# Kernel optimization log

Hardware: AMD Instinct MI355X
Metric: run time of the kernel (lower is better)

## Reference

```python
import jax, jax.numpy as jnp
import numpy as np

B, NV, HID, TDIM = 1024, 256, 256, 128
NODE_IN = 2 + 4 + TDIM  # coords + pos_enc(4) + time_emb


def _sinusoidal_pos_emb(t, dim):
    # standard SinusoidalPosEmb: cat(sin, cos) of t * exp(-i*log(1e4)/(half-1))
    half = dim // 2
    freqs = jnp.exp(-np.log(10000.0) * jnp.arange(half, dtype=t.dtype) / (half - 1))
    ang = t[:, None] * freqs[None, :]
    return jnp.concatenate([jnp.sin(ang), jnp.cos(ang)], axis=-1)  # [B, dim]


def setup_inputs() -> dict:
    key = jax.random.key(0)
    ks = jax.random.split(key, 10)
    s = lambda fan_in: 1.0 / np.sqrt(fan_in)
    return {
        "x": jax.random.normal(ks[0], (B, NV * 2), dtype=jnp.float32),
        "t": jax.random.uniform(ks[1], (B,), dtype=jnp.float32) * 1000.0,
        "time_w": jax.random.normal(ks[2], (TDIM, TDIM), dtype=jnp.float32) * s(TDIM),
        "time_b": jnp.zeros((TDIM,), dtype=jnp.float32),
        "W0": jax.random.normal(ks[3], (NODE_IN, HID), dtype=jnp.float32) * s(NODE_IN),
        "b0": jnp.zeros((HID,), dtype=jnp.float32),
        "W1": jax.random.normal(ks[4], (HID, HID), dtype=jnp.float32) * s(HID),
        "b1": jnp.zeros((HID,), dtype=jnp.float32),
        "W2": jax.random.normal(ks[5], (HID, HID), dtype=jnp.float32) * s(HID),
        "b2": jnp.zeros((HID,), dtype=jnp.float32),
    }


def reference(x, t, time_w, time_b, W0, b0, W1, b1, W2, b2):
    Bsz, D = x.shape
    n = D // 2
    coords = x.reshape(Bsz, n, 2)  # [B, n, 2]

    # cycle positional features (pos_enc_dim=4): sin/cos of vertex angle + 2nd harmonic
    pos = jnp.arange(n, dtype=x.dtype)
    theta = (2.0 * jnp.pi) * pos / n
    pe = jnp.stack([jnp.sin(theta), jnp.cos(theta), jnp.sin(2.0 * theta), jnp.cos(2.0 * theta)], axis=-1)
    pe = jnp.broadcast_to(pe[None], (Bsz, n, 4))

    # time MLP: SinusoidalPosEmb -> Linear -> SiLU, broadcast to every node of the graph
    temb = jax.nn.silu(_sinusoidal_pos_emb(t, time_w.shape[0]) @ time_w + time_b)  # [B, TDIM]
    temb = jnp.broadcast_to(temb[:, None, :], (Bsz, n, temb.shape[-1]))

    h = jnp.concatenate([coords, pe, temb], axis=-1)  # [B, n, NODE_IN]

    # GCN layers over cycle adjacency with self-loops, symmetric-normalized (deg=3 -> 1/3).
    # Cycle structure: neighbors are prev/next vertex within each polygon -> jnp.roll on axis 1.
    for W, b in ((W0, b0), (W1, b1), (W2, b2)):
        s = h @ W + b  # support = x W + b
        agg = (s + jnp.roll(s, 1, axis=1) + jnp.roll(s, -1, axis=1)) / 3.0
        h = jax.nn.silu(agg)

    # mean pooling per graph (scatter_mean over graph_index == mean over vertex axis here)
    return h.mean(axis=1)  # [B, HID]
```

## Files before the change

kernel.cpp:

```cpp
#include <hip/hip_runtime.h>
#include <cstdint>

typedef __attribute__((ext_vector_type(8)))  short bf16x8;
typedef __attribute__((ext_vector_type(16))) float f32x16;
typedef __attribute__((ext_vector_type(2)))  float f32x2;
typedef __attribute__((ext_vector_type(4)))  int   i32x4;

__device__ __forceinline__ unsigned short f2bf(float x) {
  unsigned u = __float_as_uint(x);
  u += 0x7fffu + ((u >> 16) & 1u);
  return (unsigned short)(u >> 16);
}
__device__ __forceinline__ float bf2f(unsigned short h) {
  return __uint_as_float(((unsigned)h) << 16);
}
__device__ __forceinline__ float silu_f(float v) {
  return v * __builtin_amdgcn_rcpf(1.0f + __expf(-v));
}
__device__ __forceinline__ unsigned pk2bf(float lo, float hi) {
#if defined(__has_builtin)
#if __has_builtin(__builtin_amdgcn_cvt_pk_bf16_f32)
  auto v = __builtin_amdgcn_cvt_pk_bf16_f32(lo, hi);
  unsigned u; __builtin_memcpy(&u, &v, 4); return u;
#else
  return ((unsigned)f2bf(hi) << 16) | (unsigned)f2bf(lo);
#endif
#else
  return ((unsigned)f2bf(hi) << 16) | (unsigned)f2bf(lo);
#endif
}
__device__ __forceinline__ unsigned lo_pack(unsigned x, unsigned y) {
  return __builtin_amdgcn_perm(y, x, 0x05040100u);
}
__device__ __forceinline__ unsigned hi_pack(unsigned x, unsigned y) {
  return __builtin_amdgcn_perm(y, x, 0x07060302u);
}

__global__ void pack_kernel(const float* __restrict__ W0, const float* __restrict__ W1,
                            const float* __restrict__ W2,
                            unsigned short* __restrict__ packW) {
  __shared__ float ldsF[16][257];
  const int s = blockIdx.x, tid = threadIdx.x;
  const float* W; int KT, kmax, base, kt;
  if (s < 9)       { W = W0; KT = 9;  kmax = 134; base = 0;      kt = s; }
  else if (s < 25) { W = W1; KT = 16; kmax = 256; base = 36864;  kt = s - 9; }
  else             { W = W2; KT = 16; kmax = 256; base = 102400; kt = s - 25; }
  const int k0 = kt * 16;
#pragma unroll
  for (int i = 0; i < 8; ++i) {
    const int idx = i * 512 + tid;
    const int kl = idx >> 8, col = idx & 255;
    const int kg = k0 + kl;
    ldsF[kl][col] = (kg < kmax) ? W[kg * 256 + col] : 0.0f;
  }
  __syncthreads();
  const int g = tid >> 7, t = (tid >> 6) & 1, lane = tid & 63;
  const int col = g * 64 + t * 32 + (lane & 31);
  const int kb = 8 * (lane >> 5);
  unsigned u0 = pk2bf(ldsF[kb + 0][col], ldsF[kb + 1][col]);
  unsigned u1 = pk2bf(ldsF[kb + 2][col], ldsF[kb + 3][col]);
  unsigned u2 = pk2bf(ldsF[kb + 4][col], ldsF[kb + 5][col]);
  unsigned u3 = pk2bf(ldsF[kb + 6][col], ldsF[kb + 7][col]);
  unsigned short* dst = packW + base + g * (KT * 1024) + t * (KT * 512) + kt * 512 + lane * 8;
  i32x4 v = { (int)u0, (int)u1, (int)u2, (int)u3 };
  *(i32x4*)dst = v;
}

template <int KT, int LAYER>
__device__ __forceinline__ void gcn_layer(
    const int w, const int lane, const int q, const int c, const int sig,
    const int wp, const int wn, const int ebase,
    const unsigned short* __restrict__ packL,
    const float* __restrict__ BIAS,
    const bf16x8* Aold, bf16x8* Anew,
    unsigned short* bndE, unsigned int* flagsL,
    unsigned int* scr3_w, float* poolw) {
#pragma unroll
  for (int g = 0; g < 4; ++g) {
    const int e = ebase + g;
    const unsigned short* srcg = packL + g * (KT * 1024);

    f32x16 acc0, acc1;
#pragma unroll
    for (int i = 0; i < 16; ++i) { acc0[i] = 0.f; acc1[i] = 0.f; }
    {
      const bf16x8* wb0 = (const bf16x8*)srcg;
      const bf16x8* wb1 = (const bf16x8*)(srcg + KT * 512);
#pragma unroll
      for (int kt = 0; kt < KT; ++kt) {
        bf16x8 b0 = wb0[kt * 64 + lane];
        bf16x8 b1 = wb1[kt * 64 + lane];
        acc0 = __builtin_amdgcn_mfma_f32_32x32x16_bf16(Aold[kt], b0, acc0, 0, 0, 0);
        acc1 = __builtin_amdgcn_mfma_f32_32x32x16_bf16(Aold[kt], b1, acc1, 0, 0, 0);
      }
    }

    {
      unsigned short* myb = bndE + (e * 8 + w) * 128;
      if (q == 0) { myb[c]      = f2bf(acc0[0]);  myb[32 + c] = f2bf(acc1[0]);  }
      else        { myb[64 + c] = f2bf(acc0[15]); myb[96 + c] = f2bf(acc1[15]); }
      if (lane == 0)
        __hip_atomic_store(&flagsL[e * 8 + w], 1u, __ATOMIC_RELEASE,
                           __HIP_MEMORY_SCOPE_WORKGROUP);
    }

    const float e0t0  = __shfl_xor(acc0[0], 32);
    const float e0t1  = __shfl_xor(acc1[0], 32);
    const float e15t0 = __shfl_xor(acc0[15], 32);
    const float e15t1 = __shfl_xor(acc1[15], 32);

#pragma clang loop unroll(disable)
    while (__hip_atomic_load(&flagsL[e * 8 + wp], __ATOMIC_ACQUIRE,
                             __HIP_MEMORY_SCOPE_WORKGROUP) == 0u)
      __builtin_amdgcn_s_sleep(1);
#pragma clang loop unroll(disable)
    while (__hip_atomic_load(&flagsL[e * 8 + wn], __ATOMIC_ACQUIRE,
                             __HIP_MEMORY_SCOPE_WORKGROUP) == 0u)
      __builtin_amdgcn_s_sleep(1);

    const float bp0 = bf2f(bndE[(e * 8 + wp) * 128 + 64 + c]);
    const float bp1 = bf2f(bndE[(e * 8 + wp) * 128 + 96 + c]);
    const float bn0 = bf2f(bndE[(e * 8 + wn) * 128 + c]);
    const float bn1 = bf2f(bndE[(e * 8 + wn) * 128 + 32 + c]);
    const float bias0 = BIAS[g * 64 + c], bias1 = BIAS[g * 64 + 32 + c];
    const float T = 0.33333333333f;
    float ps0 = 0.f, ps1 = 0.f;
#pragma unroll
    for (int r = 0; r < 16; ++r) {
      float pr0, pr1, nx0, nx1;
      if (r > 0)       { pr0 = acc0[r - 1]; pr1 = acc1[r - 1]; }
      else             { pr0 = q ? e15t0 : bp0; pr1 = q ? e15t1 : bp1; }
      if (r < 15)      { nx0 = acc0[r + 1]; nx1 = acc1[r + 1]; }
      else             { nx0 = q ? bn0 : e0t0; nx1 = q ? bn1 : e0t1; }
      f32x2 v2;
      v2.x = (pr0 + acc0[r] + nx0) * T + bias0;
      v2.y = (pr1 + acc1[r] + nx1) * T + bias1;
      f32x2 ex; ex.x = __expf(-v2.x); ex.y = __expf(-v2.y);
      f32x2 den = ex + 1.0f;
      f32x2 y2;
      y2.x = v2.x * __builtin_amdgcn_rcpf(den.x);
      y2.y = v2.y * __builtin_amdgcn_rcpf(den.y);
      if constexpr (LAYER == 2) { ps0 += y2.x; ps1 += y2.y; }
      else {
        scr3_w[(16 * q + r) * 34 + c] = pk2bf(y2.x, y2.y);
      }
    }

    if constexpr (LAYER == 2) {
      ps0 += __shfl_xor(ps0, 32);
      ps1 += __shfl_xor(ps1, 32);
      if (q == 0) { poolw[w * 256 + g * 64 + c]      = ps0;
                    poolw[w * 256 + g * 64 + 32 + c] = ps1; }
    } else {
      const unsigned int* sb = scr3_w + sig * 34;
      uint2 d0 = *(const uint2*)(sb + 8 * q + 0);
      uint2 d1 = *(const uint2*)(sb + 8 * q + 2);
      uint2 d2 = *(const uint2*)(sb + 8 * q + 4);
      uint2 d3 = *(const uint2*)(sb + 8 * q + 6);
      uint2 e0 = *(const uint2*)(sb + 16 + 8 * q + 0);
      uint2 e1 = *(const uint2*)(sb + 16 + 8 * q + 2);
      uint2 e2 = *(const uint2*)(sb + 16 + 8 * q + 4);
      uint2 e3 = *(const uint2*)(sb + 16 + 8 * q + 6);
      i32x4 f0 = { (int)lo_pack(d0.x, d0.y), (int)lo_pack(d1.x, d1.y),
                   (int)lo_pack(d2.x, d2.y), (int)lo_pack(d3.x, d3.y) };
      i32x4 f1 = { (int)lo_pack(e0.x, e0.y), (int)lo_pack(e1.x, e1.y),
                   (int)lo_pack(e2.x, e2.y), (int)lo_pack(e3.x, e3.y) };
      i32x4 f2v = { (int)hi_pack(d0.x, d0.y), (int)hi_pack(d1.x, d1.y),
                    (int)hi_pack(d2.x, d2.y), (int)hi_pack(d3.x, d3.y) };
      i32x4 f3 = { (int)hi_pack(e0.x, e0.y), (int)hi_pack(e1.x, e1.y),
                   (int)hi_pack(e2.x, e2.y), (int)hi_pack(e3.x, e3.y) };
      Anew[g * 4 + 0] = __builtin_bit_cast(bf16x8, f0);
      Anew[g * 4 + 1] = __builtin_bit_cast(bf16x8, f1);
      Anew[g * 4 + 2] = __builtin_bit_cast(bf16x8, f2v);
      Anew[g * 4 + 3] = __builtin_bit_cast(bf16x8, f3);
    }
  }
}

__global__ __launch_bounds__(512, 2) void poly_kernel(
    const float* __restrict__ x, const float* __restrict__ t,
    const float* __restrict__ tw, const float* __restrict__ tb,
    const unsigned short* __restrict__ packW,
    const float* __restrict__ B0, const float* __restrict__ B1,
    const float* __restrict__ B2, float* __restrict__ out) {
  __shared__ __align__(16) unsigned short bndE[12288];
  __shared__ unsigned int flagsL[96];
  __shared__ __align__(16) unsigned int   scr3[8 * 1088];
  __shared__ float poolL[2048];
  __shared__ __align__(16) unsigned short temb_sh[160];

  const int tid = threadIdx.x;
  const int w = tid >> 6, lane = tid & 63;
  const int q = lane >> 5, c = lane & 31;
  const int wp = (w + 7) & 7, wn = (w + 1) & 7;
  const int b = blockIdx.x;
  const int sig = (c & 3) + 4 * ((c >> 3) & 3) + 16 * ((c >> 2) & 1);

  if (lane < 12) flagsL[lane * 8 + w] = 0;

  {
    float* e_sh = (float*)bndE;
    float* part = (float*)scr3;
    if (tid < 128) {
      const float tv = t[b];
      const int i = tid & 63;
      const float f = expf(-0.14619588396823767f * (float)i);
      const float ang = tv * f;
      e_sh[tid] = (tid < 64) ? sinf(ang) : cosf(ang);
    }
    __syncthreads();
    {
      const int j = tid & 127, p = tid >> 7;
      float a = 0.f;
#pragma unroll 8
      for (int kk = 0; kk < 32; ++kk) {
        const int k = p * 32 + kk;
        a += e_sh[k] * tw[k * 128 + j];
      }
      part[tid] = a;
    }
    __syncthreads();
    if (tid < 128) {
      const float a = tb[tid] + part[tid] + part[128 + tid] + part[256 + tid] + part[384 + tid];
      temb_sh[6 + tid] = f2bf(silu_f(a));
      if (tid < 6)  temb_sh[tid] = 0;
      if (tid < 10) temb_sh[134 + tid] = 0;
    }
    __syncthreads();
  }

  bf16x8 A0[9], A1[16], A2[16];
  {
#pragma unroll
    for (int kt = 0; kt < 9; ++kt)
      A0[kt] = *(const bf16x8*)(temb_sh + kt * 16 + q * 8);
    if (q == 0) {
      const int n = w * 32 + sig;
      const float2 xy = ((const float2*)x)[b * 256 + n];
      const float th = 0.024543692605870074f * (float)n;
      A0[0][0] = (short)f2bf(xy.x);
      A0[0][1] = (short)f2bf(xy.y);
      A0[0][2] = (short)f2bf(sinf(th));
      A0[0][3] = (short)f2bf(cosf(th));
      A0[0][4] = (short)f2bf(sinf(2.f * th));
      A0[0][5] = (short)f2bf(cosf(2.f * th));
    }
  }

  unsigned int* scr3_w = scr3 + w * 1088;
  gcn_layer< 9, 0>(w, lane, q, c, sig, wp, wn, 0, packW,          B0, A0, A1,
                   bndE, flagsL, scr3_w, poolL);
  gcn_layer<16, 1>(w, lane, q, c, sig, wp, wn, 4, packW + 36864,  B1, A1, A2,
                   bndE, flagsL, scr3_w, poolL);
  gcn_layer<16, 2>(w, lane, q, c, sig, wp, wn, 8, packW + 102400, B2, A2, A1,
                   bndE, flagsL, scr3_w, poolL);

  __syncthreads();
  if (tid < 256) {
    float s = 0.f;
#pragma unroll
    for (int ww = 0; ww < 8; ++ww) s += poolL[ww * 256 + tid];
    out[b * 256 + tid] = s * (1.f / 256.f);
  }
}

extern "C" void kernel_launch(void* const* d_in, const int* in_sizes, int n_in,
                              void* d_out, int out_size, void* d_ws, size_t ws_size,
                              hipStream_t stream) {
  const float* x  = (const float*)d_in[0];
  const float* t  = (const float*)d_in[1];
  const float* tw = (const float*)d_in[2];
  const float* tb = (const float*)d_in[3];
  const float* W0 = (const float*)d_in[4];
  const float* b0 = (const float*)d_in[5];
  const float* W1 = (const float*)d_in[6];
  const float* b1 = (const float*)d_in[7];
  const float* W2 = (const float*)d_in[8];
  const float* b2 = (const float*)d_in[9];

  unsigned short* packW = (unsigned short*)d_ws;
  float* out = (float*)d_out;

  pack_kernel<<<41, 512, 0, stream>>>(W0, W1, W2, packW);
  poly_kernel<<<1024, 512, 0, stream>>>(x, t, tw, tb, packW, b0, b1, b2, out);
}
```

Measured before the change: 211.1 us.

## Software-pipeline GCN epilogue of previous column group with next group's MFMAs

Restructures each GCN layer so the stencil/SiLU epilogue of column group g-1 is interleaved with the MFMA k-loop of group g, using double-buffered accumulators. Weight B-fragments are also prefetched two k-steps ahead. The aim is to hide epilogue ALU/transcendental work and LDS boundary exchange behind matrix-core latency. In exchange it holds two sets of accumulators live, which raises VGPR pressure under launch_bounds(512,2) and risks spills or lower occupancy.

```diff
diff --git a/kernel.cpp b/kernel.cpp
--- a/kernel.cpp
+++ b/kernel.cpp
@@ -3,7 +3,6 @@
 
 typedef __attribute__((ext_vector_type(8)))  short bf16x8;
 typedef __attribute__((ext_vector_type(16))) float f32x16;
-typedef __attribute__((ext_vector_type(2)))  float f32x2;
 typedef __attribute__((ext_vector_type(4)))  int   i32x4;
 
 __device__ __forceinline__ unsigned short f2bf(float x) {
@@ -13,9 +12,6 @@
 }
 __device__ __forceinline__ float bf2f(unsigned short h) {
   return __uint_as_float(((unsigned)h) << 16);
-}
-__device__ __forceinline__ float silu_f(float v) {
-  return v * __builtin_amdgcn_rcpf(1.0f + __expf(-v));
 }
 __device__ __forceinline__ unsigned pk2bf(float lo, float hi) {
 #if defined(__has_builtin)
@@ -29,6 +25,9 @@
   return ((unsigned)f2bf(hi) << 16) | (unsigned)f2bf(lo);
 #endif
 }
+__device__ __forceinline__ float silu_f(float v) {
+  return v * __builtin_amdgcn_rcpf(1.0f + __expf(-v));
+}
 __device__ __forceinline__ unsigned lo_pack(unsigned x, unsigned y) {
   return __builtin_amdgcn_perm(y, x, 0x05040100u);
 }
@@ -66,6 +65,10 @@
   *(i32x4*)dst = v;
 }
 
+struct EpiPre {
+  float e0t0, e0t1, e15t0, e15t1, bp0, bp1, bn0, bn1, bias0, bias1;
+};
+
 template <int KT, int LAYER>
 __device__ __forceinline__ void gcn_layer(
     const int w, const int lane, const int q, const int c, const int sig,
@@ -75,82 +78,54 @@
     const bf16x8* Aold, bf16x8* Anew,
     unsigned short* bndE, unsigned int* flagsL,
     unsigned int* scr3_w, float* poolw) {
-#pragma unroll
-  for (int g = 0; g < 4; ++g) {
-    const int e = ebase + g;
-    const unsigned short* srcg = packL + g * (KT * 1024);
-
-    f32x16 acc0, acc1;
-#pragma unroll
-    for (int i = 0; i < 16; ++i) { acc0[i] = 0.f; acc1[i] = 0.f; }
-    {
-      const bf16x8* wb0 = (const bf16x8*)srcg;
-      const bf16x8* wb1 = (const bf16x8*)(srcg + KT * 512);
-#pragma unroll
-      for (int kt = 0; kt < KT; ++kt) {
-        bf16x8 b0 = wb0[kt * 64 + lane];
-        bf16x8 b1 = wb1[kt * 64 + lane];
-        acc0 = __builtin_amdgcn_mfma_f32_32x32x16_bf16(Aold[kt], b0, acc0, 0, 0, 0);
-        acc1 = __builtin_amdgcn_mfma_f32_32x32x16_bf16(Aold[kt], b1, acc1, 0, 0, 0);
-      }
-    }
-
-    {
-      unsigned short* myb = bndE + (e * 8 + w) * 128;
-      if (q == 0) { myb[c]      = f2bf(acc0[0]);  myb[32 + c] = f2bf(acc1[0]);  }
-      else        { myb[64 + c] = f2bf(acc0[15]); myb[96 + c] = f2bf(acc1[15]); }
-      if (lane == 0)
-        __hip_atomic_store(&flagsL[e * 8 + w], 1u, __ATOMIC_RELEASE,
-                           __HIP_MEMORY_SCOPE_WORKGROUP);
-    }
-
-    const float e0t0  = __shfl_xor(acc0[0], 32);
-    const float e0t1  = __shfl_xor(acc1[0], 32);
-    const float e15t0 = __shfl_xor(acc0[15], 32);
-    const float e15t1 = __shfl_xor(acc1[15], 32);
-
-#pragma clang loop unroll(disable)
-    while (__hip_atomic_load(&flagsL[e * 8 + wp], __ATOMIC_ACQUIRE,
+  const float T = 0.33333333333f;
+  f32x16 a0[2], a1[2];
+  EpiPre ep;
+  float ps0 = 0.f, ps1 = 0.f;
+
+  auto spin = [&](int ww, int e) {
+    while (__hip_atomic_load(&flagsL[e * 8 + ww], __ATOMIC_ACQUIRE,
                              __HIP_MEMORY_SCOPE_WORKGROUP) == 0u)
       __builtin_amdgcn_s_sleep(1);
-#pragma clang loop unroll(disable)
-    while (__hip_atomic_load(&flagsL[e * 8 + wn], __ATOMIC_ACQUIRE,
-                             __HIP_MEMORY_SCOPE_WORKGROUP) == 0u)
-      __builtin_amdgcn_s_sleep(1);
-
-    const float bp0 = bf2f(bndE[(e * 8 + wp) * 128 + 64 + c]);
-    const float bp1 = bf2f(bndE[(e * 8 + wp) * 128 + 96 + c]);
-    const float bn0 = bf2f(bndE[(e * 8 + wn) * 128 + c]);
-    const float bn1 = bf2f(bndE[(e * 8 + wn) * 128 + 32 + c]);
-    const float bias0 = BIAS[g * 64 + c], bias1 = BIAS[g * 64 + 32 + c];
-    const float T = 0.33333333333f;
-    float ps0 = 0.f, ps1 = 0.f;
-#pragma unroll
-    for (int r = 0; r < 16; ++r) {
-      float pr0, pr1, nx0, nx1;
-      if (r > 0)       { pr0 = acc0[r - 1]; pr1 = acc1[r - 1]; }
-      else             { pr0 = q ? e15t0 : bp0; pr1 = q ? e15t1 : bp1; }
-      if (r < 15)      { nx0 = acc0[r + 1]; nx1 = acc1[r + 1]; }
-      else             { nx0 = q ? bn0 : e0t0; nx1 = q ? bn1 : e0t1; }
-      f32x2 v2;
-      v2.x = (pr0 + acc0[r] + nx0) * T + bias0;
-      v2.y = (pr1 + acc1[r] + nx1) * T + bias1;
-      f32x2 ex; ex.x = __expf(-v2.x); ex.y = __expf(-v2.y);
-      f32x2 den = ex + 1.0f;
-      f32x2 y2;
-      y2.x = v2.x * __builtin_amdgcn_rcpf(den.x);
-      y2.y = v2.y * __builtin_amdgcn_rcpf(den.y);
-      if constexpr (LAYER == 2) { ps0 += y2.x; ps1 += y2.y; }
-      else {
-        scr3_w[(16 * q + r) * 34 + c] = pk2bf(y2.x, y2.y);
-      }
-    }
-
+  };
+  auto publish = [&](int g, const f32x16& C0, const f32x16& C1) {
+    unsigned short* myb = bndE + ((ebase + g) * 8 + w) * 128;
+    if (q == 0) { myb[c]      = f2bf(C0[0]);  myb[32 + c] = f2bf(C1[0]);  }
+    else        { myb[64 + c] = f2bf(C0[15]); myb[96 + c] = f2bf(C1[15]); }
+    if (lane == 0)
+      __hip_atomic_store(&flagsL[(ebase + g) * 8 + w], 1u, __ATOMIC_RELEASE,
+                         __HIP_MEMORY_SCOPE_WORKGROUP);
+  };
+  auto epi_prep = [&](int pg, const f32x16& P0, const f32x16& P1) {
+    const int e = ebase + pg;
+    ep.e0t0  = __shfl_xor(P0[0], 32);  ep.e0t1  = __shfl_xor(P1[0], 32);
+    ep.e15t0 = __shfl_xor(P0[15], 32); ep.e15t1 = __shfl_xor(P1[15], 32);
+    ep.bp0 = bf2f(bndE[(e * 8 + wp) * 128 + 64 + c]);
+    ep.bp1 = bf2f(bndE[(e * 8 + wp) * 128 + 96 + c]);
+    ep.bn0 = bf2f(bndE[(e * 8 + wn) * 128 + c]);
+    ep.bn1 = bf2f(bndE[(e * 8 + wn) * 128 + 32 + c]);
+    ep.bias0 = BIAS[pg * 64 + c]; ep.bias1 = BIAS[pg * 64 + 32 + c];
+    ps0 = 0.f; ps1 = 0.f;
+  };
+  auto epi_iter = [&](int r, const f32x16& P0, const f32x16& P1) {
+    float pr0, pr1, nx0, nx1;
+    if (r > 0)  { pr0 = P0[r - 1]; pr1 = P1[r - 1]; }
+    else        { pr0 = q ? ep.e15t0 : ep.bp0; pr1 = q ? ep.e15t1 : ep.bp1; }
+    if (r < 15) { nx0 = P0[r + 1]; nx1 = P1[r + 1]; }
+    else        { nx0 = q ? ep.bn0 : ep.e0t0; nx1 = q ? ep.bn1 : ep.e0t1; }
+    const float v0 = (pr0 + P0[r] + nx0) * T + ep.bias0;
+    const float v1 = (pr1 + P1[r] + nx1) * T + ep.bias1;
+    const float y0 = silu_f(v0);
+    const float y1 = silu_f(v1);
+    if constexpr (LAYER == 2) { ps0 += y0; ps1 += y1; }
+    else scr3_w[(16 * q + r) * 34 + c] = pk2bf(y0, y1);
+  };
+  auto epi_fini = [&](int pg) {
     if constexpr (LAYER == 2) {
-      ps0 += __shfl_xor(ps0, 32);
-      ps1 += __shfl_xor(ps1, 32);
-      if (q == 0) { poolw[w * 256 + g * 64 + c]      = ps0;
-                    poolw[w * 256 + g * 64 + 32 + c] = ps1; }
+      float s0 = ps0 + __shfl_xor(ps0, 32);
+      float s1 = ps1 + __shfl_xor(ps1, 32);
+      if (q == 0) { poolw[w * 256 + pg * 64 + c]      = s0;
+                    poolw[w * 256 + pg * 64 + 32 + c] = s1; }
     } else {
       const unsigned int* sb = scr3_w + sig * 34;
       uint2 d0 = *(const uint2*)(sb + 8 * q + 0);
@@ -169,12 +144,52 @@
                     (int)hi_pack(d2.x, d2.y), (int)hi_pack(d3.x, d3.y) };
       i32x4 f3 = { (int)hi_pack(e0.x, e0.y), (int)hi_pack(e1.x, e1.y),
                    (int)hi_pack(e2.x, e2.y), (int)hi_pack(e3.x, e3.y) };
-      Anew[g * 4 + 0] = __builtin_bit_cast(bf16x8, f0);
-      Anew[g * 4 + 1] = __builtin_bit_cast(bf16x8, f1);
-      Anew[g * 4 + 2] = __builtin_bit_cast(bf16x8, f2v);
-      Anew[g * 4 + 3] = __builtin_bit_cast(bf16x8, f3);
-    }
-  }
+      Anew[pg * 4 + 0] = __builtin_bit_cast(bf16x8, f0);
+      Anew[pg * 4 + 1] = __builtin_bit_cast(bf16x8, f1);
+      Anew[pg * 4 + 2] = __builtin_bit_cast(bf16x8, f2v);
+      Anew[pg * 4 + 3] = __builtin_bit_cast(bf16x8, f3);
+    }
+  };
+  auto run_group = [&](int g, f32x16& C0, f32x16& C1,
+                       const f32x16& P0, const f32x16& P1, bool doEpi) {
+    const bf16x8* wb0 = (const bf16x8*)(packL + g * (KT * 1024));
+    const bf16x8* wb1 = (const bf16x8*)(packL + g * (KT * 1024) + KT * 512);
+#pragma unroll
+    for (int i = 0; i < 16; ++i) { C0[i] = 0.f; C1[i] = 0.f; }
+    bf16x8 pb0[2], pb1[2];
+    pb0[0] = wb0[lane]; pb1[0] = wb1[lane];
+    if (KT > 1) { pb0[1] = wb0[64 + lane]; pb1[1] = wb1[64 + lane]; }
+#pragma unroll
+    for (int kt = 0; kt < KT; ++kt) {
+      bf16x8 b0 = pb0[kt & 1], b1 = pb1[kt & 1];
+      if (kt + 2 < KT) { pb0[kt & 1] = wb0[(kt + 2) * 64 + lane];
+                         pb1[kt & 1] = wb1[(kt + 2) * 64 + lane]; }
+      C0 = __builtin_amdgcn_mfma_f32_32x32x16_bf16(Aold[kt], b0, C0, 0, 0, 0);
+      C1 = __builtin_amdgcn_mfma_f32_32x32x16_bf16(Aold[kt], b1, C1, 0, 0, 0);
+      if (doEpi) {
+#pragma unroll
+        for (int r = (kt * 16) / KT; r < ((kt + 1) * 16) / KT; ++r)
+          epi_iter(r, P0, P1);
+      }
+    }
+  };
+
+  run_group(0, a0[0], a1[0], a0[0], a1[0], false);
+  publish(0, a0[0], a1[0]);
+#pragma unroll
+  for (int g = 1; g <= 3; ++g) {
+    const int pg = g - 1, pp = pg & 1, cp = g & 1;
+    spin(wp, ebase + pg); spin(wn, ebase + pg);
+    epi_prep(pg, a0[pp], a1[pp]);
+    run_group(g, a0[cp], a1[cp], a0[pp], a1[pp], true);
+    epi_fini(pg);
+    publish(g, a0[cp], a1[cp]);
+  }
+  spin(wp, ebase + 3); spin(wn, ebase + 3);
+  epi_prep(3, a0[1], a1[1]);
+#pragma unroll
+  for (int r = 0; r < 16; ++r) epi_iter(r, a0[1], a1[1]);
+  epi_fini(3);
 }
 
 __global__ __launch_bounds__(512, 2) void poly_kernel(
```

New measurement: 201.9 us. -4.3%, faster.

## Compute all output column tiles per layer at once with one neighbor sync

Applied to the files above, without the earlier changes.

Each GCN layer now issues MFMAs for all eight 32-column tiles in a single k-loop, holding eight accumulators instead of two per column group. The prev/next boundary rows are then exchanged through LDS with one flag handshake per layer instead of four. The weight pack layout is reordered to match this k-major, tile-inner order. The layer-1 activations are rewritten in place, and the pooling buffer and time-embedding scratch now reuse the boundary LDS region, which cuts register arrays and LDS footprint. The cost is 128 accumulator floats live per lane, which may cause spills or lower occupancy under the 512x2 launch bounds.

```diff
diff --git a/kernel.cpp b/kernel.cpp
--- a/kernel.cpp
+++ b/kernel.cpp
@@ -3,7 +3,6 @@
 
 typedef __attribute__((ext_vector_type(8)))  short bf16x8;
 typedef __attribute__((ext_vector_type(16))) float f32x16;
-typedef __attribute__((ext_vector_type(2)))  float f32x2;
 typedef __attribute__((ext_vector_type(4)))  int   i32x4;
 
 __device__ __forceinline__ unsigned short f2bf(float x) {
@@ -13,9 +12,6 @@
 }
 __device__ __forceinline__ float bf2f(unsigned short h) {
   return __uint_as_float(((unsigned)h) << 16);
-}
-__device__ __forceinline__ float silu_f(float v) {
-  return v * __builtin_amdgcn_rcpf(1.0f + __expf(-v));
 }
 __device__ __forceinline__ unsigned pk2bf(float lo, float hi) {
 #if defined(__has_builtin)
@@ -29,6 +25,9 @@
   return ((unsigned)f2bf(hi) << 16) | (unsigned)f2bf(lo);
 #endif
 }
+__device__ __forceinline__ float silu_f(float v) {
+  return v * __builtin_amdgcn_rcpf(1.0f + __expf(-v));
+}
 __device__ __forceinline__ unsigned lo_pack(unsigned x, unsigned y) {
   return __builtin_amdgcn_perm(y, x, 0x05040100u);
 }
@@ -41,10 +40,10 @@
                             unsigned short* __restrict__ packW) {
   __shared__ float ldsF[16][257];
   const int s = blockIdx.x, tid = threadIdx.x;
-  const float* W; int KT, kmax, base, kt;
-  if (s < 9)       { W = W0; KT = 9;  kmax = 134; base = 0;      kt = s; }
-  else if (s < 25) { W = W1; KT = 16; kmax = 256; base = 36864;  kt = s - 9; }
-  else             { W = W2; KT = 16; kmax = 256; base = 102400; kt = s - 25; }
+  const float* W; int kmax, base, kt;
+  if (s < 9)       { W = W0; kmax = 134; base = 0;      kt = s; }
+  else if (s < 25) { W = W1; kmax = 256; base = 36864;  kt = s - 9; }
+  else             { W = W2; kmax = 256; base = 102400; kt = s - 25; }
   const int k0 = kt * 16;
 #pragma unroll
   for (int i = 0; i < 8; ++i) {
@@ -54,103 +53,101 @@
     ldsF[kl][col] = (kg < kmax) ? W[kg * 256 + col] : 0.0f;
   }
   __syncthreads();
-  const int g = tid >> 7, t = (tid >> 6) & 1, lane = tid & 63;
-  const int col = g * 64 + t * 32 + (lane & 31);
+  const int j = tid >> 6, lane = tid & 63;
+  const int col = j * 32 + (lane & 31);
   const int kb = 8 * (lane >> 5);
-  unsigned u0 = pk2bf(ldsF[kb + 0][col], ldsF[kb + 1][col]);
-  unsigned u1 = pk2bf(ldsF[kb + 2][col], ldsF[kb + 3][col]);
-  unsigned u2 = pk2bf(ldsF[kb + 4][col], ldsF[kb + 5][col]);
-  unsigned u3 = pk2bf(ldsF[kb + 6][col], ldsF[kb + 7][col]);
-  unsigned short* dst = packW + base + g * (KT * 1024) + t * (KT * 512) + kt * 512 + lane * 8;
-  i32x4 v = { (int)u0, (int)u1, (int)u2, (int)u3 };
-  *(i32x4*)dst = v;
+  i32x4 v = { (int)pk2bf(ldsF[kb + 0][col], ldsF[kb + 1][col]),
+              (int)pk2bf(ldsF[kb + 2][col], ldsF[kb + 3][col]),
+              (int)pk2bf(ldsF[kb + 4][col], ldsF[kb + 5][col]),
+              (int)pk2bf(ldsF[kb + 6][col], ldsF[kb + 7][col]) };
+  *(i32x4*)(packW + base + (kt * 8 + j) * 512 + lane * 8) = v;
 }
 
 template <int KT, int LAYER>
 __device__ __forceinline__ void gcn_layer(
     const int w, const int lane, const int q, const int c, const int sig,
-    const int wp, const int wn, const int ebase,
+    const int wp, const int wn, const int e,
     const unsigned short* __restrict__ packL,
     const float* __restrict__ BIAS,
     const bf16x8* Aold, bf16x8* Anew,
     unsigned short* bndE, unsigned int* flagsL,
     unsigned int* scr3_w, float* poolw) {
-#pragma unroll
-  for (int g = 0; g < 4; ++g) {
-    const int e = ebase + g;
-    const unsigned short* srcg = packL + g * (KT * 1024);
-
-    f32x16 acc0, acc1;
-#pragma unroll
-    for (int i = 0; i < 16; ++i) { acc0[i] = 0.f; acc1[i] = 0.f; }
-    {
-      const bf16x8* wb0 = (const bf16x8*)srcg;
-      const bf16x8* wb1 = (const bf16x8*)(srcg + KT * 512);
-#pragma unroll
-      for (int kt = 0; kt < KT; ++kt) {
-        bf16x8 b0 = wb0[kt * 64 + lane];
-        bf16x8 b1 = wb1[kt * 64 + lane];
-        acc0 = __builtin_amdgcn_mfma_f32_32x32x16_bf16(Aold[kt], b0, acc0, 0, 0, 0);
-        acc1 = __builtin_amdgcn_mfma_f32_32x32x16_bf16(Aold[kt], b1, acc1, 0, 0, 0);
+  const float T = 0.33333333333f;
+  f32x16 acc[8];
+#pragma unroll
+  for (int j = 0; j < 8; ++j)
+#pragma unroll
+    for (int i = 0; i < 16; ++i) acc[j][i] = 0.f;
+
+  {
+    const bf16x8* wb = (const bf16x8*)packL;
+#pragma unroll
+    for (int kt = 0; kt < KT; ++kt) {
+#pragma unroll
+      for (int j = 0; j < 8; ++j) {
+        bf16x8 bf = wb[(kt * 8 + j) * 64 + lane];
+        acc[j] = __builtin_amdgcn_mfma_f32_32x32x16_bf16(Aold[kt], bf, acc[j], 0, 0, 0);
       }
     }
-
-    {
-      unsigned short* myb = bndE + (e * 8 + w) * 128;
-      if (q == 0) { myb[c]      = f2bf(acc0[0]);  myb[32 + c] = f2bf(acc1[0]);  }
-      else        { myb[64 + c] = f2bf(acc0[15]); myb[96 + c] = f2bf(acc1[15]); }
-      if (lane == 0)
-        __hip_atomic_store(&flagsL[e * 8 + w], 1u, __ATOMIC_RELEASE,
-                           __HIP_MEMORY_SCOPE_WORKGROUP);
-    }
-
-    const float e0t0  = __shfl_xor(acc0[0], 32);
-    const float e0t1  = __shfl_xor(acc1[0], 32);
-    const float e15t0 = __shfl_xor(acc0[15], 32);
-    const float e15t1 = __shfl_xor(acc1[15], 32);
-
+  }
+
+  {
+    unsigned short* myb = bndE + (e * 8 + w) * 512;
+    if (q == 0) {
+#pragma unroll
+      for (int j = 0; j < 8; ++j) myb[j * 32 + c] = f2bf(acc[j][0]);
+    } else {
+#pragma unroll
+      for (int j = 0; j < 8; ++j) myb[256 + j * 32 + c] = f2bf(acc[j][15]);
+    }
+    if (lane == 0)
+      __hip_atomic_store(&flagsL[e * 8 + w], 1u, __ATOMIC_RELEASE,
+                         __HIP_MEMORY_SCOPE_WORKGROUP);
+  }
 #pragma clang loop unroll(disable)
-    while (__hip_atomic_load(&flagsL[e * 8 + wp], __ATOMIC_ACQUIRE,
-                             __HIP_MEMORY_SCOPE_WORKGROUP) == 0u)
-      __builtin_amdgcn_s_sleep(1);
+  while (__hip_atomic_load(&flagsL[e * 8 + wp], __ATOMIC_ACQUIRE,
+                           __HIP_MEMORY_SCOPE_WORKGROUP) == 0u)
+    __builtin_amdgcn_s_sleep(1);
 #pragma clang loop unroll(disable)
-    while (__hip_atomic_load(&flagsL[e * 8 + wn], __ATOMIC_ACQUIRE,
-                             __HIP_MEMORY_SCOPE_WORKGROUP) == 0u)
-      __builtin_amdgcn_s_sleep(1);
-
-    const float bp0 = bf2f(bndE[(e * 8 + wp) * 128 + 64 + c]);
-    const float bp1 = bf2f(bndE[(e * 8 + wp) * 128 + 96 + c]);
-    const float bn0 = bf2f(bndE[(e * 8 + wn) * 128 + c]);
-    const float bn1 = bf2f(bndE[(e * 8 + wn) * 128 + 32 + c]);
-    const float bias0 = BIAS[g * 64 + c], bias1 = BIAS[g * 64 + 32 + c];
-    const float T = 0.33333333333f;
+  while (__hip_atomic_load(&flagsL[e * 8 + wn], __ATOMIC_ACQUIRE,
+                           __HIP_MEMORY_SCOPE_WORKGROUP) == 0u)
+    __builtin_amdgcn_s_sleep(1);
+
+  const unsigned short* pb = bndE + (e * 8 + wp) * 512 + 256;
+  const unsigned short* nb = bndE + (e * 8 + wn) * 512;
+
+#pragma unroll
+  for (int cg = 0; cg < 4; ++cg) {
+    const int j0 = 2 * cg, j1 = 2 * cg + 1;
+    const float e0t0  = __shfl_xor(acc[j0][0], 32);
+    const float e0t1  = __shfl_xor(acc[j1][0], 32);
+    const float e15t0 = __shfl_xor(acc[j0][15], 32);
+    const float e15t1 = __shfl_xor(acc[j1][15], 32);
+    const float bp0 = bf2f(pb[j0 * 32 + c]);
+    const float bp1 = bf2f(pb[j1 * 32 + c]);
+    const float bn0 = bf2f(nb[j0 * 32 + c]);
+    const float bn1 = bf2f(nb[j1 * 32 + c]);
+    const float bias0 = BIAS[j0 * 32 + c], bias1 = BIAS[j1 * 32 + c];
     float ps0 = 0.f, ps1 = 0.f;
 #pragma unroll
     for (int r = 0; r < 16; ++r) {
       float pr0, pr1, nx0, nx1;
-      if (r > 0)       { pr0 = acc0[r - 1]; pr1 = acc1[r - 1]; }
-      else             { pr0 = q ? e15t0 : bp0; pr1 = q ? e15t1 : bp1; }
-      if (r < 15)      { nx0 = acc0[r + 1]; nx1 = acc1[r + 1]; }
-      else             { nx0 = q ? bn0 : e0t0; nx1 = q ? bn1 : e0t1; }
-      f32x2 v2;
-      v2.x = (pr0 + acc0[r] + nx0) * T + bias0;
-      v2.y = (pr1 + acc1[r] + nx1) * T + bias1;
-      f32x2 ex; ex.x = __expf(-v2.x); ex.y = __expf(-v2.y);
-      f32x2 den = ex + 1.0f;
-      f32x2 y2;
-      y2.x = v2.x * __builtin_amdgcn_rcpf(den.x);
-      y2.y = v2.y * __builtin_amdgcn_rcpf(den.y);
-      if constexpr (LAYER == 2) { ps0 += y2.x; ps1 += y2.y; }
-      else {
-        scr3_w[(16 * q + r) * 34 + c] = pk2bf(y2.x, y2.y);
-      }
-    }
-
+      if (r > 0)  { pr0 = acc[j0][r - 1]; pr1 = acc[j1][r - 1]; }
+      else        { pr0 = q ? e15t0 : bp0; pr1 = q ? e15t1 : bp1; }
+      if (r < 15) { nx0 = acc[j0][r + 1]; nx1 = acc[j1][r + 1]; }
+      else        { nx0 = q ? bn0 : e0t0; nx1 = q ? bn1 : e0t1; }
+      const float v0 = (pr0 + acc[j0][r] + nx0) * T + bias0;
+      const float v1 = (pr1 + acc[j1][r] + nx1) * T + bias1;
+      const float y0 = silu_f(v0);
+      const float y1 = silu_f(v1);
+      if constexpr (LAYER == 2) { ps0 += y0; ps1 += y1; }
+      else scr3_w[(16 * q + r) * 34 + c] = pk2bf(y0, y1);
+    }
     if constexpr (LAYER == 2) {
-      ps0 += __shfl_xor(ps0, 32);
-      ps1 += __shfl_xor(ps1, 32);
-      if (q == 0) { poolw[w * 256 + g * 64 + c]      = ps0;
-                    poolw[w * 256 + g * 64 + 32 + c] = ps1; }
+      float s0 = ps0 + __shfl_xor(ps0, 32);
+      float s1 = ps1 + __shfl_xor(ps1, 32);
+      if (q == 0) { poolw[w * 256 + cg * 64 + c]      = s0;
+                    poolw[w * 256 + cg * 64 + 32 + c] = s1; }
     } else {
       const unsigned int* sb = scr3_w + sig * 34;
       uint2 d0 = *(const uint2*)(sb + 8 * q + 0);
@@ -169,10 +166,10 @@
                     (int)hi_pack(d2.x, d2.y), (int)hi_pack(d3.x, d3.y) };
       i32x4 f3 = { (int)hi_pack(e0.x, e0.y), (int)hi_pack(e1.x, e1.y),
                    (int)hi_pack(e2.x, e2.y), (int)hi_pack(e3.x, e3.y) };
-      Anew[g * 4 + 0] = __builtin_bit_cast(bf16x8, f0);
-      Anew[g * 4 + 1] = __builtin_bit_cast(bf16x8, f1);
-      Anew[g * 4 + 2] = __builtin_bit_cast(bf16x8, f2v);
-      Anew[g * 4 + 3] = __builtin_bit_cast(bf16x8, f3);
+      Anew[cg * 4 + 0] = __builtin_bit_cast(bf16x8, f0);
+      Anew[cg * 4 + 1] = __builtin_bit_cast(bf16x8, f1);
+      Anew[cg * 4 + 2] = __builtin_bit_cast(bf16x8, f2v);
+      Anew[cg * 4 + 3] = __builtin_bit_cast(bf16x8, f3);
     }
   }
 }
@@ -184,10 +181,10 @@
     const float* __restrict__ B0, const float* __restrict__ B1,
     const float* __restrict__ B2, float* __restrict__ out) {
   __shared__ __align__(16) unsigned short bndE[12288];
-  __shared__ unsigned int flagsL[96];
+  __shared__ unsigned int flagsL[24];
   __shared__ __align__(16) unsigned int   scr3[8 * 1088];
-  __shared__ float poolL[2048];
   __shared__ __align__(16) unsigned short temb_sh[160];
+  float* poolL = (float*)bndE;
 
   const int tid = threadIdx.x;
   const int w = tid >> 6, lane = tid & 63;
@@ -196,10 +193,10 @@
   const int b = blockIdx.x;
   const int sig = (c & 3) + 4 * ((c >> 3) & 3) + 16 * ((c >> 2) & 1);
 
-  if (lane < 12) flagsL[lane * 8 + w] = 0;
-
-  {
-    float* e_sh = (float*)bndE;
+  if (lane < 3) flagsL[lane * 8 + w] = 0;
+
+  {
+    float* e_sh = (float*)(bndE + 4096);
     float* part = (float*)scr3;
     if (tid < 128) {
       const float tv = t[b];
@@ -229,7 +226,7 @@
     __syncthreads();
   }
 
-  bf16x8 A0[9], A1[16], A2[16];
+  bf16x8 A0[9], A1[16];
   {
 #pragma unroll
     for (int kt = 0; kt < 9; ++kt)
@@ -250,9 +247,9 @@
   unsigned int* scr3_w = scr3 + w * 1088;
   gcn_layer< 9, 0>(w, lane, q, c, sig, wp, wn, 0, packW,          B0, A0, A1,
                    bndE, flagsL, scr3_w, poolL);
-  gcn_layer<16, 1>(w, lane, q, c, sig, wp, wn, 4, packW + 36864,  B1, A1, A2,
+  gcn_layer<16, 1>(w, lane, q, c, sig, wp, wn, 1, packW + 36864,  B1, A1, A1,
                    bndE, flagsL, scr3_w, poolL);
-  gcn_layer<16, 2>(w, lane, q, c, sig, wp, wn, 8, packW + 102400, B2, A2, A1,
+  gcn_layer<16, 2>(w, lane, q, c, sig, wp, wn, 2, packW + 102400, B2, A1, A1,
                    bndE, flagsL, scr3_w, poolL);
 
   __syncthreads();
```

After: 319.8 us. +51.5%, slower.

## Replace flag spin-waits with double-buffered barrier exchange, prefetch weights, fold SiLU constants

Applied to the files above, without the earlier changes.

Each GCN group's neighbour-boundary exchange now uses a double-buffered LDS array of packed bf16 pairs and a single __syncthreads, replacing per-wave release/acquire flags and sleep-polling. This removes the flag and bndE LDS arrays and lets the pooling buffer alias the scratch array. The first weight fragment of the next group is prefetched into registers while the current group's epilogue runs. SiLU is rewritten with exp2 and pre-folded log2e, 1/3 and bias constants using paired float ops. The workgroup-wide barrier makes every wave wait for the slowest one in each group, where the old scheme only waited on the two neighbours.

```diff
diff --git a/kernel.cpp b/kernel.cpp
--- a/kernel.cpp
+++ b/kernel.cpp
@@ -13,9 +13,6 @@
 }
 __device__ __forceinline__ float bf2f(unsigned short h) {
   return __uint_as_float(((unsigned)h) << 16);
-}
-__device__ __forceinline__ float silu_f(float v) {
-  return v * __builtin_amdgcn_rcpf(1.0f + __expf(-v));
 }
 __device__ __forceinline__ unsigned pk2bf(float lo, float hi) {
 #if defined(__has_builtin)
@@ -28,6 +25,20 @@
 #else
   return ((unsigned)f2bf(hi) << 16) | (unsigned)f2bf(lo);
 #endif
+}
+__device__ __forceinline__ float exp2_f(float x) {
+#if defined(__has_builtin)
+#if __has_builtin(__builtin_amdgcn_exp2f)
+  return __builtin_amdgcn_exp2f(x);
+#else
+  return __builtin_exp2f(x);
+#endif
+#else
+  return __builtin_exp2f(x);
+#endif
+}
+__device__ __forceinline__ float silu_f(float v) {
+  return v * __builtin_amdgcn_rcpf(1.0f + __expf(-v));
 }
 __device__ __forceinline__ unsigned lo_pack(unsigned x, unsigned y) {
   return __builtin_amdgcn_perm(y, x, 0x05040100u);
@@ -69,25 +80,30 @@
 template <int KT, int LAYER>
 __device__ __forceinline__ void gcn_layer(
     const int w, const int lane, const int q, const int c, const int sig,
-    const int wp, const int wn, const int ebase,
     const unsigned short* __restrict__ packL,
     const float* __restrict__ BIAS,
     const bf16x8* Aold, bf16x8* Anew,
-    unsigned short* bndE, unsigned int* flagsL,
-    unsigned int* scr3_w, float* poolw) {
+    unsigned int* bndu, unsigned int* scr3_w, float* poolw) {
+  const float T  = 0.33333333333f;
+  const float L2E = 1.44269504f;
+  const float NL2 = -0.69314718f;
+
+  bf16x8 pf0 = ((const bf16x8*)packL)[lane];
+  bf16x8 pf1 = ((const bf16x8*)(packL + KT * 512))[lane];
+
 #pragma unroll
   for (int g = 0; g < 4; ++g) {
-    const int e = ebase + g;
     const unsigned short* srcg = packL + g * (KT * 1024);
-
     f32x16 acc0, acc1;
 #pragma unroll
     for (int i = 0; i < 16; ++i) { acc0[i] = 0.f; acc1[i] = 0.f; }
     {
       const bf16x8* wb0 = (const bf16x8*)srcg;
       const bf16x8* wb1 = (const bf16x8*)(srcg + KT * 512);
-#pragma unroll
-      for (int kt = 0; kt < KT; ++kt) {
+      acc0 = __builtin_amdgcn_mfma_f32_32x32x16_bf16(Aold[0], pf0, acc0, 0, 0, 0);
+      acc1 = __builtin_amdgcn_mfma_f32_32x32x16_bf16(Aold[0], pf1, acc1, 0, 0, 0);
+#pragma unroll
+      for (int kt = 1; kt < KT; ++kt) {
         bf16x8 b0 = wb0[kt * 64 + lane];
         bf16x8 b1 = wb1[kt * 64 + lane];
         acc0 = __builtin_amdgcn_mfma_f32_32x32x16_bf16(Aold[kt], b0, acc0, 0, 0, 0);
@@ -95,62 +111,55 @@
       }
     }
 
-    {
-      unsigned short* myb = bndE + (e * 8 + w) * 128;
-      if (q == 0) { myb[c]      = f2bf(acc0[0]);  myb[32 + c] = f2bf(acc1[0]);  }
-      else        { myb[64 + c] = f2bf(acc0[15]); myb[96 + c] = f2bf(acc1[15]); }
-      if (lane == 0)
-        __hip_atomic_store(&flagsL[e * 8 + w], 1u, __ATOMIC_RELEASE,
-                           __HIP_MEMORY_SCOPE_WORKGROUP);
-    }
+    if (g < 3) {
+      const unsigned short* nxt = packL + (g + 1) * (KT * 1024);
+      pf0 = ((const bf16x8*)nxt)[lane];
+      pf1 = ((const bf16x8*)(nxt + KT * 512))[lane];
+    }
+
+    unsigned int* bndp = bndu + (g & 1) * 1024;
+    if (q == 0) bndp[(w * 2 + 0) * 32 + c] = pk2bf(acc0[0],  acc1[0]);
+    else        bndp[(w * 2 + 1) * 32 + c] = pk2bf(acc0[15], acc1[15]);
+    __syncthreads();
 
     const float e0t0  = __shfl_xor(acc0[0], 32);
     const float e0t1  = __shfl_xor(acc1[0], 32);
     const float e15t0 = __shfl_xor(acc0[15], 32);
     const float e15t1 = __shfl_xor(acc1[15], 32);
-
-#pragma clang loop unroll(disable)
-    while (__hip_atomic_load(&flagsL[e * 8 + wp], __ATOMIC_ACQUIRE,
-                             __HIP_MEMORY_SCOPE_WORKGROUP) == 0u)
-      __builtin_amdgcn_s_sleep(1);
-#pragma clang loop unroll(disable)
-    while (__hip_atomic_load(&flagsL[e * 8 + wn], __ATOMIC_ACQUIRE,
-                             __HIP_MEMORY_SCOPE_WORKGROUP) == 0u)
-      __builtin_amdgcn_s_sleep(1);
-
-    const float bp0 = bf2f(bndE[(e * 8 + wp) * 128 + 64 + c]);
-    const float bp1 = bf2f(bndE[(e * 8 + wp) * 128 + 96 + c]);
-    const float bn0 = bf2f(bndE[(e * 8 + wn) * 128 + c]);
-    const float bn1 = bf2f(bndE[(e * 8 + wn) * 128 + 32 + c]);
+    const unsigned pbu = bndp[(((w + 7) & 7) * 2 + 1) * 32 + c];
+    const unsigned nbu = bndp[(((w + 1) & 7) * 2 + 0) * 32 + c];
+    const float bp0 = bf2f((unsigned short)(pbu & 0xffff));
+    const float bp1 = bf2f((unsigned short)(pbu >> 16));
+    const float bn0 = bf2f((unsigned short)(nbu & 0xffff));
+    const float bn1 = bf2f((unsigned short)(nbu >> 16));
     const float bias0 = BIAS[g * 64 + c], bias1 = BIAS[g * 64 + 32 + c];
-    const float T = 0.33333333333f;
-    float ps0 = 0.f, ps1 = 0.f;
+    f32x2 cT2;  cT2.x = -L2E * T;      cT2.y = -L2E * T;
+    f32x2 nb2;  nb2.x = -L2E * bias0;  nb2.y = -L2E * bias1;
+    f32x2 ps2;  ps2.x = 0.f;           ps2.y = 0.f;
 #pragma unroll
     for (int r = 0; r < 16; ++r) {
-      float pr0, pr1, nx0, nx1;
-      if (r > 0)       { pr0 = acc0[r - 1]; pr1 = acc1[r - 1]; }
-      else             { pr0 = q ? e15t0 : bp0; pr1 = q ? e15t1 : bp1; }
-      if (r < 15)      { nx0 = acc0[r + 1]; nx1 = acc1[r + 1]; }
-      else             { nx0 = q ? bn0 : e0t0; nx1 = q ? bn1 : e0t1; }
-      f32x2 v2;
-      v2.x = (pr0 + acc0[r] + nx0) * T + bias0;
-      v2.y = (pr1 + acc1[r] + nx1) * T + bias1;
-      f32x2 ex; ex.x = __expf(-v2.x); ex.y = __expf(-v2.y);
-      f32x2 den = ex + 1.0f;
-      f32x2 y2;
-      y2.x = v2.x * __builtin_amdgcn_rcpf(den.x);
-      y2.y = v2.y * __builtin_amdgcn_rcpf(den.y);
-      if constexpr (LAYER == 2) { ps0 += y2.x; ps1 += y2.y; }
-      else {
-        scr3_w[(16 * q + r) * 34 + c] = pk2bf(y2.x, y2.y);
-      }
+      f32x2 pr2, nx2, ac2;
+      if (r > 0)  { pr2.x = acc0[r - 1]; pr2.y = acc1[r - 1]; }
+      else        { pr2.x = q ? e15t0 : bp0; pr2.y = q ? e15t1 : bp1; }
+      if (r < 15) { nx2.x = acc0[r + 1]; nx2.y = acc1[r + 1]; }
+      else        { nx2.x = q ? bn0 : e0t0; nx2.y = q ? bn1 : e0t1; }
+      ac2.x = acc0[r]; ac2.y = acc1[r];
+      f32x2 s2 = (pr2 + ac2) + nx2;
+      f32x2 n2 = s2 * cT2 + nb2;
+      f32x2 v2 = n2 * NL2;
+      f32x2 e2; e2.x = exp2_f(n2.x); e2.y = exp2_f(n2.y);
+      f32x2 d2 = e2 + 1.0f;
+      f32x2 r2; r2.x = __builtin_amdgcn_rcpf(d2.x); r2.y = __builtin_amdgcn_rcpf(d2.y);
+      f32x2 y2 = v2 * r2;
+      if constexpr (LAYER == 2) { ps2 += y2; }
+      else scr3_w[(16 * q + r) * 34 + c] = pk2bf(y2.x, y2.y);
     }
 
     if constexpr (LAYER == 2) {
-      ps0 += __shfl_xor(ps0, 32);
-      ps1 += __shfl_xor(ps1, 32);
-      if (q == 0) { poolw[w * 256 + g * 64 + c]      = ps0;
-                    poolw[w * 256 + g * 64 + 32 + c] = ps1; }
+      float s0 = ps2.x + __shfl_xor(ps2.x, 32);
+      float s1 = ps2.y + __shfl_xor(ps2.y, 32);
+      if (q == 0) { poolw[w * 256 + g * 64 + c]      = s0;
+                    poolw[w * 256 + g * 64 + 32 + c] = s1; }
     } else {
       const unsigned int* sb = scr3_w + sig * 34;
       uint2 d0 = *(const uint2*)(sb + 8 * q + 0);
@@ -183,23 +192,18 @@
     const unsigned short* __restrict__ packW,
     const float* __restrict__ B0, const float* __restrict__ B1,
     const float* __restrict__ B2, float* __restrict__ out) {
-  __shared__ __align__(16) unsigned short bndE[12288];
-  __shared__ unsigned int flagsL[96];
+  __shared__ __align__(16) unsigned int   bndu[2048];
   __shared__ __align__(16) unsigned int   scr3[8 * 1088];
-  __shared__ float poolL[2048];
   __shared__ __align__(16) unsigned short temb_sh[160];
 
   const int tid = threadIdx.x;
   const int w = tid >> 6, lane = tid & 63;
   const int q = lane >> 5, c = lane & 31;
-  const int wp = (w + 7) & 7, wn = (w + 1) & 7;
   const int b = blockIdx.x;
   const int sig = (c & 3) + 4 * ((c >> 3) & 3) + 16 * ((c >> 2) & 1);
 
-  if (lane < 12) flagsL[lane * 8 + w] = 0;
-
   {
-    float* e_sh = (float*)bndE;
+    float* e_sh = (float*)bndu;
     float* part = (float*)scr3;
     if (tid < 128) {
       const float tv = t[b];
@@ -248,18 +252,16 @@
   }
 
   unsigned int* scr3_w = scr3 + w * 1088;
-  gcn_layer< 9, 0>(w, lane, q, c, sig, wp, wn, 0, packW,          B0, A0, A1,
-                   bndE, flagsL, scr3_w, poolL);
-  gcn_layer<16, 1>(w, lane, q, c, sig, wp, wn, 4, packW + 36864,  B1, A1, A2,
-                   bndE, flagsL, scr3_w, poolL);
-  gcn_layer<16, 2>(w, lane, q, c, sig, wp, wn, 8, packW + 102400, B2, A2, A1,
-                   bndE, flagsL, scr3_w, poolL);
+  float* poolw = (float*)scr3;
+  gcn_layer< 9, 0>(w, lane, q, c, sig, packW,          B0, A0, A1, bndu, scr3_w, poolw);
+  gcn_layer<16, 1>(w, lane, q, c, sig, packW + 36864,  B1, A1, A2, bndu, scr3_w, poolw);
+  gcn_layer<16, 2>(w, lane, q, c, sig, packW + 102400, B2, A2, A1, bndu, scr3_w, poolw);
 
   __syncthreads();
   if (tid < 256) {
     float s = 0.f;
 #pragma unroll
-    for (int ww = 0; ww < 8; ++ww) s += poolL[ww * 256 + tid];
+    for (int ww = 0; ww < 8; ++ww) s += poolw[ww * 256 + tid];
     out[b * 256 + tid] = s * (1.f / 256.f);
   }
 }
```

Measured after the change: 208.1 us. Within noise of the previous version (-1.4%).
